# Performance work log

Measured on AMD Instinct MI355X. Metric: run time of the kernel, lower is better.

The kernel has to match this reference:

```python
import jax, jax.numpy as jnp
import numpy as np

N_HEAD = 12


def setup_inputs() -> dict:
    key = jax.random.key(0)
    k1, k2, k3 = jax.random.split(key, 3)
    B, T, C = 1, 4096, 768
    x = jax.random.normal(k1, (B, T, C), dtype=jnp.float32)
    w_attn = jax.random.normal(k2, (C, 3 * C), dtype=jnp.float32) * (1.0 / np.sqrt(C))
    w_proj = jax.random.normal(k3, (C, C), dtype=jnp.float32) * (1.0 / np.sqrt(C))
    return {"x": x, "w_attn": w_attn, "w_proj": w_proj}


def reference(x, w_attn, w_proj):
    B, T, C = x.shape
    hd = C // N_HEAD
    qkv = x @ w_attn  # [B, T, 3C]
    q, k, v = jnp.split(qkv, 3, axis=-1)
    # [B, H, T, hd]
    q = q.reshape(B, T, N_HEAD, hd).transpose(0, 2, 1, 3)
    k = k.reshape(B, T, N_HEAD, hd).transpose(0, 2, 1, 3)
    v = v.reshape(B, T, N_HEAD, hd).transpose(0, 2, 1, 3)
    scale = 1.0 / np.sqrt(hd).astype(np.float32)
    att = jnp.einsum('bhtd,bhsd->bhts', q, k) * scale  # materialized TxT scores
    causal = jnp.tril(jnp.ones((T, T), dtype=bool))
    att = jnp.where(causal[None, None], att, -jnp.inf)
    att = jax.nn.softmax(att, axis=-1)
    y = jnp.einsum('bhts,bhsd->bhtd', att, v)  # [B, H, T, hd]
    y = y.transpose(0, 2, 1, 3).reshape(B, T, C)
    return y @ w_proj
```

## Files before the change

kernel.cpp:

```cpp
#include <hip/hip_runtime.h>


typedef short bf16x8 __attribute__((ext_vector_type(8)));
typedef float f32x4 __attribute__((ext_vector_type(4)));

#define T_SEQ 4096
#define C_DIM 768
#define NH 12
#define HD 64

__device__ __forceinline__ unsigned short f2bf(float f) {
  union { float f; unsigned u; } v; v.f = f;
  unsigned r = v.u + 0x7FFFu + ((v.u >> 16) & 1u);
  return (unsigned short)(r >> 16);
}
__device__ __forceinline__ float bf2f(unsigned short u) {
  union { unsigned u; float f; } v; v.u = ((unsigned)u) << 16;
  return v.f;
}
__device__ __forceinline__ unsigned cvtpk(float a, float b) {
  unsigned r;
  asm("v_cvt_pk_bf16_f32 %0, %1, %2" : "=v"(r) : "v"(a), "v"(b));
  return r;
}
#define E2(x) __builtin_amdgcn_exp2f(x)

#define GLD16(g, l) __builtin_amdgcn_global_load_lds( \
    (const __attribute__((address_space(1))) void*)(g), \
    (__attribute__((address_space(3))) void*)(l), 16, 0, 0)

__device__ __forceinline__ void tr_body(const float* __restrict__ in,
                                        unsigned short* __restrict__ out,
                                        int R, int Cc, int bx, int by,
                                        float (*tile)[33]) {
  int tx = threadIdx.x & 31, ty = threadIdx.x >> 5;
#pragma unroll
  for (int i = 0; i < 32; i += 8)
    tile[ty + i][tx] = in[(size_t)(by * 32 + ty + i) * Cc + bx * 32 + tx];
  __syncthreads();
#pragma unroll
  for (int i = 0; i < 32; i += 8)
    out[(size_t)(bx * 32 + ty + i) * R + by * 32 + tx] = f2bf(tile[tx][ty + i]);
}

__global__ void prep(const float* __restrict__ x, unsigned short* __restrict__ Xb,
                     const float* __restrict__ w_attn, unsigned short* __restrict__ WaT,
                     const float* __restrict__ w_proj, unsigned short* __restrict__ WpT) {
  __shared__ float tile[32][33];
  const int bid = blockIdx.x;
  if (bid < 3072) {
    int i = (bid * 256 + threadIdx.x) * 4;
    float4 v = *reinterpret_cast<const float4*>(x + i);
    ushort4 o;
    o.x = f2bf(v.x); o.y = f2bf(v.y); o.z = f2bf(v.z); o.w = f2bf(v.w);
    *reinterpret_cast<ushort4*>(Xb + i) = o;
  } else if (bid < 3072 + 1728) {
    int b = bid - 3072;
    tr_body(w_attn, WaT, 768, 2304, b % 72, b / 72, tile);
  } else {
    int b = bid - 4800;
    tr_body(w_proj, WpT, 768, 768, b % 24, b / 24, tile);
  }
}

template <int MODE>
__global__ __launch_bounds__(256, 4)
void gemm_bt(const unsigned short* __restrict__ A,
             const unsigned short* __restrict__ Bt,
             void* __restrict__ out0,
             unsigned short* __restrict__ Kout,
             unsigned short* __restrict__ Vt,
             int M, int N, int K) {
  __shared__ __align__(16) unsigned short As[128 * 64];
  __shared__ __align__(16) unsigned short Bs[64 * 64];
  const int nbn = N / 64;
  const int nwg = (M / 128) * nbn;
  const int cpx = nwg >> 3;
  const int swz = ((int)blockIdx.x & 7) * cpx + ((int)blockIdx.x >> 3);
  const int bm = swz / nbn, bn = swz % nbn;
  const int tid = threadIdx.x;
  const int wid = tid >> 6, lane = tid & 63;
  const int wr = wid >> 1, wc = wid & 1;
  const int lr = lane & 15;
  const int lk8 = (lane >> 4) * 8;
  const int rsub = lane >> 3, csub = (lane & 7) * 8;

  f32x4 acc[4][2] = {};

  const int nk = K / 64;
  for (int kt = 0; kt < nk; ++kt) {
    __syncthreads();
    {
      const unsigned short* gA = A + (size_t)(bm * 128) * K + kt * 64;
      const unsigned short* gB = Bt + (size_t)(bn * 64) * K + kt * 64;
#pragma unroll
      for (int c = 0; c < 4; ++c) {
        int seg = wid * 4 + c;
        int row = seg * 8 + rsub;
        GLD16(gA + (size_t)row * K + csub, (char*)As + seg * 1024);
      }
#pragma unroll
      for (int c = 0; c < 2; ++c) {
        int seg = wid * 2 + c;
        int row = seg * 8 + rsub;
        GLD16(gB + (size_t)row * K + csub, (char*)Bs + seg * 1024);
      }
    }
    __syncthreads();
#pragma unroll
    for (int kk = 0; kk < 2; ++kk) {
      bf16x8 a[4], b[2];
      int lk = kk * 32 + lk8;
#pragma unroll
      for (int m = 0; m < 4; ++m)
        a[m] = *reinterpret_cast<const bf16x8*>(&As[(wr * 64 + m * 16 + lr) * 64 + lk]);
#pragma unroll
      for (int n = 0; n < 2; ++n)
        b[n] = *reinterpret_cast<const bf16x8*>(&Bs[(wc * 32 + n * 16 + lr) * 64 + lk]);
#pragma unroll
      for (int m = 0; m < 4; ++m)
#pragma unroll
        for (int n = 0; n < 2; ++n)
          acc[m][n] = __builtin_amdgcn_mfma_f32_16x16x32_bf16(a[m], b[n], acc[m][n], 0, 0, 0);
    }
  }

  const int row0 = bm * 128 + wr * 64;
  const int col0 = bn * 64 + wc * 32;
#pragma unroll
  for (int m = 0; m < 4; ++m)
#pragma unroll
    for (int n = 0; n < 2; ++n)
#pragma unroll
      for (int j = 0; j < 4; ++j) {
        int r = row0 + m * 16 + (lane >> 4) * 4 + j;
        int c = col0 + n * 16 + (lane & 15);
        float v = acc[m][n][j];
        if (MODE == 0) {
          if (c < 768)
            ((unsigned short*)out0)[(size_t)r * 768 + c] = f2bf(v * 0.180336884f);
          else if (c < 1536)
            Kout[(size_t)r * 768 + (c - 768)] = f2bf(v);
          else
            Vt[(size_t)(c - 1536) * M + r] = f2bf(v);
        } else {
          ((float*)out0)[(size_t)r * N + c] = v;
        }
      }
}

__device__ __forceinline__ void stage_kv(const unsigned short* __restrict__ Kb,
                                         const unsigned short* __restrict__ Vt,
                                         unsigned short* Kbuf, unsigned short* Vbuf,
                                         int h, int st, int wid, int lane) {
  const int cg = lane & 7, rsub = (lane >> 3) & 7;
  const unsigned short* gK = Kb + (size_t)(st * 64) * C_DIM + h * 64;
  const unsigned short* gV = Vt + (size_t)(h * 64) * T_SEQ + st * 64;
#pragma unroll
  for (int c = 0; c < 2; ++c) {
    int seg = wid * 2 + c;
    int row = seg * 8 + rsub;
    GLD16(gK + (size_t)row * C_DIM + (cg ^ rsub) * 8, (char*)Kbuf + seg * 1024);
    GLD16(gV + (size_t)row * T_SEQ + (cg ^ rsub) * 8, (char*)Vbuf + seg * 1024);
  }
}

__device__ __forceinline__ int part_off(int qb) {
  return (qb < 16) ? (qb - 8) * 2 : (qb < 24) ? 16 + (qb - 16) * 3 : 40 + (qb - 24) * 4;
}
__device__ __forceinline__ unsigned short* part_ptr(char* pA, char* pB, int set) {
  return (set < 768) ? (unsigned short*)(pA + (size_t)set * 16384)
                     : (unsigned short*)(pB + (size_t)(set - 768) * 16384);
}

__global__ __launch_bounds__(256, 3)
void attn_fwd(const unsigned short* __restrict__ Qb,
              const unsigned short* __restrict__ Kb,
              const unsigned short* __restrict__ Vt,
              unsigned short* __restrict__ Y,
              char* __restrict__ partA, char* __restrict__ partB,
              float* __restrict__ ml) {
  __shared__ __align__(16) unsigned short Ks[2][64 * 64];
  __shared__ __align__(16) unsigned short Vs[2][64 * 64];
  __shared__ __align__(16) unsigned short Ps[4][32 * 64];

  const int h = blockIdx.x;
  int qb = 0, ck = 0;
  {
    int idx = blockIdx.y;
    for (int q = 31; q >= 0; --q) {
      int nc = q / 8 + 1;
      if (idx < nc) { qb = q; ck = idx; break; }
      idx -= nc;
    }
  }
  const int nch = qb / 8 + 1;
  const int q0 = qb * 128;
  const int nst_total = q0 / 64 + 2;
  const int st0 = ck * 16;
  const int st1 = (st0 + 16 < nst_total) ? st0 + 16 : nst_total;

  const int tid = threadIdx.x;
  const int wid = tid >> 6, lane = tid & 63;
  const int l15 = lane & 15, g = lane >> 4;
  const int sw = l15 & 7;
  const int qw = q0 + wid * 32;

  bf16x8 qf[2][2];
#pragma unroll
  for (int m = 0; m < 2; ++m)
#pragma unroll
    for (int kk = 0; kk < 2; ++kk)
      qf[m][kk] = *reinterpret_cast<const bf16x8*>(
          &Qb[(size_t)(qw + m * 16 + l15) * C_DIM + h * 64 + kk * 32 + g * 8]);

  f32x4 o[2][4] = {};
  float mrow[2] = {-1e30f, -1e30f};
  float lsum[2] = {0.f, 0.f};

  stage_kv(Kb, Vt, Ks[0], Vs[0], h, st0, wid, lane);
  int cur = 0;

  for (int st = st0; st < st1; ++st) {
    if (st + 1 < st1) {
      stage_kv(Kb, Vt, Ks[cur ^ 1], Vs[cur ^ 1], h, st + 1, wid, lane);
      asm volatile("s_waitcnt vmcnt(4)" ::: "memory");
    } else {
      asm volatile("s_waitcnt vmcnt(0)" ::: "memory");
    }
    __builtin_amdgcn_s_barrier();

    const bool active = (st * 64) <= (qw + 31);
    if (active) {
      const unsigned short* K_ = Ks[cur];
      const unsigned short* V_ = Vs[cur];

      f32x4 sT[2][4] = {};
      __builtin_amdgcn_s_setprio(1);
#pragma unroll
      for (int kk = 0; kk < 2; ++kk) {
        bf16x8 kf[4];
#pragma unroll
        for (int n = 0; n < 4; ++n)
          kf[n] = *reinterpret_cast<const bf16x8*>(
              &K_[(n * 16 + l15) * 64 + (((kk * 4 + g) ^ sw) * 8)]);
#pragma unroll
        for (int m = 0; m < 2; ++m)
#pragma unroll
          for (int n = 0; n < 4; ++n)
            sT[m][n] = __builtin_amdgcn_mfma_f32_16x16x32_bf16(kf[n], qf[m][kk], sT[m][n], 0, 0, 0);
      }
      __builtin_amdgcn_s_setprio(0);

      unsigned short* Pw = Ps[wid];
#pragma unroll
      for (int m = 0; m < 2; ++m) {
        float vmax = -1e30f;
        if (st * 64 + 63 <= qw + m * 16) {
#pragma unroll
          for (int n = 0; n < 4; ++n)
#pragma unroll
            for (int jj = 0; jj < 4; ++jj) vmax = fmaxf(vmax, sT[m][n][jj]);
        } else {
          const int bound = (qw + m * 16 + l15) - st * 64;
#pragma unroll
          for (int n = 0; n < 4; ++n)
#pragma unroll
            for (int jj = 0; jj < 4; ++jj) {
              int sl = n * 16 + g * 4 + jj;
              float v = sT[m][n][jj];
              v = (sl <= bound) ? v : -1e30f;
              sT[m][n][jj] = v;
              vmax = fmaxf(vmax, v);
            }
        }
        vmax = fmaxf(vmax, __shfl_xor(vmax, 16, 64));
        vmax = fmaxf(vmax, __shfl_xor(vmax, 32, 64));
        const bool defer = (__all(vmax <= mrow[m] + 8.0f) != 0);
        const float mnew = defer ? mrow[m] : fmaxf(mrow[m], vmax);
        float ps = 0.f;
#pragma unroll
        for (int n = 0; n < 4; ++n)
#pragma unroll
          for (int jj = 0; jj < 4; ++jj) {
            float p = E2(sT[m][n][jj] - mnew);
            sT[m][n][jj] = p;
            ps += p;
          }
        ps += __shfl_xor(ps, 16, 64);
        ps += __shfl_xor(ps, 32, 64);
        if (defer) {
          lsum[m] += ps;
        } else {
          float alpha = E2(mrow[m] - mnew);
          lsum[m] = lsum[m] * alpha + ps;
          mrow[m] = mnew;
#pragma unroll
          for (int n2 = 0; n2 < 4; ++n2) o[m][n2] *= alpha;
        }
#pragma unroll
        for (int n = 0; n < 4; ++n) {
          uint2 pw;
          pw.x = cvtpk(sT[m][n][0], sT[m][n][1]);
          pw.y = cvtpk(sT[m][n][2], sT[m][n][3]);
          *reinterpret_cast<uint2*>(
              &Pw[(m * 16 + l15) * 64 + (((n * 2 + (g >> 1)) ^ sw) * 8) + (g & 1) * 4]) = pw;
        }
      }
      asm volatile("s_waitcnt lgkmcnt(0)" ::: "memory");

      __builtin_amdgcn_s_setprio(1);
#pragma unroll
      for (int ks = 0; ks < 2; ++ks) {
        bf16x8 vf[4], pf[2];
#pragma unroll
        for (int n2 = 0; n2 < 4; ++n2)
          vf[n2] = *reinterpret_cast<const bf16x8*>(
              &V_[(n2 * 16 + l15) * 64 + (((ks * 4 + g) ^ sw) * 8)]);
#pragma unroll
        for (int m = 0; m < 2; ++m)
          pf[m] = *reinterpret_cast<const bf16x8*>(
              &Pw[(m * 16 + l15) * 64 + (((ks * 4 + g) ^ sw) * 8)]);
#pragma unroll
        for (int m = 0; m < 2; ++m)
#pragma unroll
          for (int n2 = 0; n2 < 4; ++n2)
            o[m][n2] = __builtin_amdgcn_mfma_f32_16x16x32_bf16(vf[n2], pf[m], o[m][n2], 0, 0, 0);
      }
      __builtin_amdgcn_s_setprio(0);
    }
    asm volatile("" ::: "memory");
    __builtin_amdgcn_s_barrier();
    cur ^= 1;
  }

  if (nch == 1) {
#pragma unroll
    for (int m = 0; m < 2; ++m) {
      float inv = 1.0f / lsum[m];
      int qg = qw + m * 16 + l15;
#pragma unroll
      for (int n2 = 0; n2 < 4; ++n2) {
        uint2 yk;
        yk.x = cvtpk(o[m][n2][0] * inv, o[m][n2][1] * inv);
        yk.y = cvtpk(o[m][n2][2] * inv, o[m][n2][3] * inv);
        *reinterpret_cast<uint2*>(&Y[(size_t)qg * C_DIM + h * 64 + n2 * 16 + g * 4]) = yk;
      }
    }
  } else {
    const int set = h * 72 + part_off(qb) + ck;
    unsigned short* po = part_ptr(partA, partB, set);
#pragma unroll
    for (int m = 0; m < 2; ++m) {
      int qL = wid * 32 + m * 16 + l15;
#pragma unroll
      for (int n2 = 0; n2 < 4; ++n2) {
        uint2 pk;
        pk.x = cvtpk(o[m][n2][0], o[m][n2][1]);
        pk.y = cvtpk(o[m][n2][2], o[m][n2][3]);
        *reinterpret_cast<uint2*>(&po[qL * 64 + n2 * 16 + g * 4]) = pk;
      }
      if (g == 0) {
        ml[(size_t)set * 256 + qL * 2] = mrow[m];
        ml[(size_t)set * 256 + qL * 2 + 1] = lsum[m];
      }
    }
  }
}

__global__ __launch_bounds__(256)
void attn_combine(char* __restrict__ partA, char* __restrict__ partB,
                  const float* __restrict__ ml, unsigned short* __restrict__ Y) {
  const int qb = 8 + blockIdx.x;
  const int h = blockIdx.y;
  const int nch = qb / 8 + 1;
  const int set0 = h * 72 + part_off(qb);
  const int t = threadIdx.x;
  const int r = t >> 1, dh = (t & 1) * 32;

  float mi[4], li[4];
  float M = -1e30f;
  for (int i = 0; i < nch; ++i) {
    mi[i] = ml[(size_t)(set0 + i) * 256 + r * 2];
    li[i] = ml[(size_t)(set0 + i) * 256 + r * 2 + 1];
    M = fmaxf(M, mi[i]);
  }
  float L = 0.f;
  float O[32];
#pragma unroll
  for (int d = 0; d < 32; ++d) O[d] = 0.f;
  for (int i = 0; i < nch; ++i) {
    float w = E2(mi[i] - M);
    L += li[i] * w;
    const unsigned short* po = part_ptr(partA, partB, set0 + i) + r * 64 + dh;
#pragma unroll
    for (int d4 = 0; d4 < 32; d4 += 4) {
      ushort4 v = *reinterpret_cast<const ushort4*>(po + d4);
      O[d4 + 0] += bf2f(v.x) * w;
      O[d4 + 1] += bf2f(v.y) * w;
      O[d4 + 2] += bf2f(v.z) * w;
      O[d4 + 3] += bf2f(v.w) * w;
    }
  }
  float inv = 1.0f / L;
  unsigned short* yp = Y + (size_t)(qb * 128 + r) * C_DIM + h * 64 + dh;
#pragma unroll
  for (int d4 = 0; d4 < 32; d4 += 4) {
    uint2 yk;
    yk.x = cvtpk(O[d4 + 0] * inv, O[d4 + 1] * inv);
    yk.y = cvtpk(O[d4 + 2] * inv, O[d4 + 3] * inv);
    *reinterpret_cast<uint2*>(yp + d4) = yk;
  }
}

extern "C" void kernel_launch(void* const* d_in, const int* in_sizes, int n_in,
                              void* d_out, int out_size, void* d_ws, size_t ws_size,
                              hipStream_t stream) {
  const float* x = (const float*)d_in[0];
  const float* w_attn = (const float*)d_in[1];
  const float* w_proj = (const float*)d_in[2];
  float* out = (float*)d_out;

  char* ws = (char*)d_ws;
  unsigned short* Xb   = (unsigned short*)(ws + 0);
  unsigned short* WaT  = (unsigned short*)(ws + 6291456);
  unsigned short* WpT  = (unsigned short*)(ws + 9830400);
  unsigned short* Qb   = (unsigned short*)(ws + 11010048);
  unsigned short* Kb   = (unsigned short*)(ws + 17301504);
  unsigned short* Vt   = (unsigned short*)(ws + 23592960);
  unsigned short* Yb   = (unsigned short*)(ws + 29884416);

  char* partA = (char*)d_out;
  char* partB = (char*)ws;
  float* mlp  = (float*)(ws + 6291456);

  prep<<<5376, 256, 0, stream>>>(x, Xb, w_attn, WaT, w_proj, WpT);

  gemm_bt<0><<<(T_SEQ / 128) * (2304 / 64), 256, 0, stream>>>(
      Xb, WaT, (void*)Qb, Kb, Vt, T_SEQ, 2304, C_DIM);

  attn_fwd<<<dim3(NH, 80), 256, 0, stream>>>(Qb, Kb, Vt, Yb, partA, partB, mlp);
  attn_combine<<<dim3(24, NH), 256, 0, stream>>>(partA, partB, mlp, Yb);

  gemm_bt<1><<<(T_SEQ / 128) * (C_DIM / 64), 256, 0, stream>>>(
      Yb, WpT, (void*)out, nullptr, nullptr, T_SEQ, C_DIM, C_DIM);
}
```

Measured before the change: 140.8 us.

## Shrink attention KV split chunks to 12 tiles and tree-reduce softmax max/sum

Reduces the KV-chunk size per attention block from 16 to 12 key tiles, raising the grid from 80 to 102 blocks per head and adding more partial sets for the combine kernel (26 q-blocks, up to 6 chunks). This aims to improve load balance and occupancy across CUs for the causal split-K attention. It also restructures the row max and row sum into tree reductions to shorten dependency chains. The costs are more partial-result traffic and more combine work, and the partial buffers must still fit the workspace layout.

After: 138.1 us. No clear change (-1.9%).

```diff
diff --git a/kernel.cpp b/kernel.cpp
--- a/kernel.cpp
+++ b/kernel.cpp
@@ -165,8 +165,13 @@
   }
 }
 
+__device__ __forceinline__ int nchunks(int q) { return (2 * q + 13) / 12; }
 __device__ __forceinline__ int part_off(int qb) {
-  return (qb < 16) ? (qb - 8) * 2 : (qb < 24) ? 16 + (qb - 16) * 3 : 40 + (qb - 24) * 4;
+  if (qb < 12) return (qb - 6) * 2;
+  if (qb < 18) return 12 + (qb - 12) * 3;
+  if (qb < 24) return 30 + (qb - 18) * 4;
+  if (qb < 30) return 54 + (qb - 24) * 5;
+  return 84 + (qb - 30) * 6;
 }
 __device__ __forceinline__ unsigned short* part_ptr(char* pA, char* pB, int set) {
   return (set < 768) ? (unsigned short*)(pA + (size_t)set * 16384)
@@ -189,16 +194,16 @@
   {
     int idx = blockIdx.y;
     for (int q = 31; q >= 0; --q) {
-      int nc = q / 8 + 1;
+      int nc = nchunks(q);
       if (idx < nc) { qb = q; ck = idx; break; }
       idx -= nc;
     }
   }
-  const int nch = qb / 8 + 1;
+  const int nch = nchunks(qb);
   const int q0 = qb * 128;
-  const int nst_total = q0 / 64 + 2;
-  const int st0 = ck * 16;
-  const int st1 = (st0 + 16 < nst_total) ? st0 + 16 : nst_total;
+  const int nst_total = 2 * qb + 2;
+  const int st0 = ck * 12;
+  const int st1 = (st0 + 12 < nst_total) ? st0 + 12 : nst_total;
 
   const int tid = threadIdx.x;
   const int wid = tid >> 6, lane = tid & 63;
@@ -255,38 +260,35 @@
       unsigned short* Pw = Ps[wid];
 #pragma unroll
       for (int m = 0; m < 2; ++m) {
-        float vmax = -1e30f;
-        if (st * 64 + 63 <= qw + m * 16) {
-#pragma unroll
-          for (int n = 0; n < 4; ++n)
-#pragma unroll
-            for (int jj = 0; jj < 4; ++jj) vmax = fmaxf(vmax, sT[m][n][jj]);
-        } else {
+        if (!(st * 64 + 63 <= qw + m * 16)) {
           const int bound = (qw + m * 16 + l15) - st * 64;
 #pragma unroll
           for (int n = 0; n < 4; ++n)
 #pragma unroll
             for (int jj = 0; jj < 4; ++jj) {
               int sl = n * 16 + g * 4 + jj;
-              float v = sT[m][n][jj];
-              v = (sl <= bound) ? v : -1e30f;
-              sT[m][n][jj] = v;
-              vmax = fmaxf(vmax, v);
+              if (sl > bound) sT[m][n][jj] = -1e30f;
             }
         }
+        float vm[4];
+#pragma unroll
+        for (int n = 0; n < 4; ++n)
+          vm[n] = fmaxf(fmaxf(sT[m][n][0], sT[m][n][1]), fmaxf(sT[m][n][2], sT[m][n][3]));
+        float vmax = fmaxf(fmaxf(vm[0], vm[1]), fmaxf(vm[2], vm[3]));
         vmax = fmaxf(vmax, __shfl_xor(vmax, 16, 64));
         vmax = fmaxf(vmax, __shfl_xor(vmax, 32, 64));
         const bool defer = (__all(vmax <= mrow[m] + 8.0f) != 0);
         const float mnew = defer ? mrow[m] : fmaxf(mrow[m], vmax);
-        float ps = 0.f;
 #pragma unroll
         for (int n = 0; n < 4; ++n)
 #pragma unroll
-          for (int jj = 0; jj < 4; ++jj) {
-            float p = E2(sT[m][n][jj] - mnew);
-            sT[m][n][jj] = p;
-            ps += p;
-          }
+          for (int jj = 0; jj < 4; ++jj)
+            sT[m][n][jj] = E2(sT[m][n][jj] - mnew);
+        float sm[4];
+#pragma unroll
+        for (int n = 0; n < 4; ++n)
+          sm[n] = (sT[m][n][0] + sT[m][n][1]) + (sT[m][n][2] + sT[m][n][3]);
+        float ps = (sm[0] + sm[1]) + (sm[2] + sm[3]);
         ps += __shfl_xor(ps, 16, 64);
         ps += __shfl_xor(ps, 32, 64);
         if (defer) {
@@ -348,7 +350,7 @@
       }
     }
   } else {
-    const int set = h * 72 + part_off(qb) + ck;
+    const int set = h * 96 + part_off(qb) + ck;
     unsigned short* po = part_ptr(partA, partB, set);
 #pragma unroll
     for (int m = 0; m < 2; ++m) {
@@ -371,14 +373,14 @@
 __global__ __launch_bounds__(256)
 void attn_combine(char* __restrict__ partA, char* __restrict__ partB,
                   const float* __restrict__ ml, unsigned short* __restrict__ Y) {
-  const int qb = 8 + blockIdx.x;
+  const int qb = 6 + blockIdx.x;
   const int h = blockIdx.y;
-  const int nch = qb / 8 + 1;
-  const int set0 = h * 72 + part_off(qb);
+  const int nch = nchunks(qb);
+  const int set0 = h * 96 + part_off(qb);
   const int t = threadIdx.x;
   const int r = t >> 1, dh = (t & 1) * 32;
 
-  float mi[4], li[4];
+  float mi[6], li[6];
   float M = -1e30f;
   for (int i = 0; i < nch; ++i) {
     mi[i] = ml[(size_t)(set0 + i) * 256 + r * 2];
@@ -439,8 +441,8 @@
   gemm_bt<0><<<(T_SEQ / 128) * (2304 / 64), 256, 0, stream>>>(
       Xb, WaT, (void*)Qb, Kb, Vt, T_SEQ, 2304, C_DIM);
 
-  attn_fwd<<<dim3(NH, 80), 256, 0, stream>>>(Qb, Kb, Vt, Yb, partA, partB, mlp);
-  attn_combine<<<dim3(24, NH), 256, 0, stream>>>(partA, partB, mlp, Yb);
+  attn_fwd<<<dim3(NH, 102), 256, 0, stream>>>(Qb, Kb, Vt, Yb, partA, partB, mlp);
+  attn_combine<<<dim3(26, NH), 256, 0, stream>>>(partA, partB, mlp, Yb);
 
   gemm_bt<1><<<(T_SEQ / 128) * (C_DIM / 64), 256, 0, stream>>>(
       Yb, WpT, (void*)out, nullptr, nullptr, T_SEQ, C_DIM, C_DIM);
```
